# Optimization experiments

Measured on AMD Instinct MI355X. Metric: run time of the kernel, lower is better.

The kernel has to match this reference:

```python
import jax, jax.numpy as jnp
import numpy as np

OUT_CH = 300
KSIZE = 337

def setup_inputs() -> dict:
    key = jax.random.key(0)
    k1, k2, kw, kb, kf1, kb1, kf2, kb2 = jax.random.split(key, 8)
    B, W = 512, 128
    x1 = jax.random.normal(k1, (B, W, KSIZE), dtype=jnp.float32)
    x2 = jax.random.normal(k2, (B, W, KSIZE), dtype=jnp.float32)
    # Conv1d(1, 300, 337) weight [300, 1, 337] -> collapse to [300, 337]
    conv_w = jax.random.normal(kw, (OUT_CH, KSIZE), dtype=jnp.float32) * (1.0 / np.sqrt(KSIZE))
    conv_b = jax.random.normal(kb, (OUT_CH,), dtype=jnp.float32) * 0.01
    fc1_w = jax.random.normal(kf1, (300, 600), dtype=jnp.float32) * (1.0 / np.sqrt(600))
    fc1_b = jax.random.normal(kb1, (300,), dtype=jnp.float32) * 0.01
    fc2_w = jax.random.normal(kf2, (1, 300), dtype=jnp.float32) * (1.0 / np.sqrt(300))
    fc2_b = jax.random.normal(kb2, (1,), dtype=jnp.float32) * 0.01
    return {"x1": x1, "x2": x2, "conv_w": conv_w, "conv_b": conv_b,
            "fc1_w": fc1_w, "fc1_b": fc1_b, "fc2_w": fc2_w, "fc2_b": fc2_b}

def _encode(x, conv_w, conv_b):
    # per-word conv1d with full-length kernel == matmul over last dim
    # x: [B, W, 337] -> [B, W, 300] -> relu -> max over words -> [B, 300]
    h = jnp.einsum('bwd,od->bwo', x, conv_w) + conv_b
    h = jax.nn.relu(h)
    return jnp.max(h, axis=1)

def reference(x1, x2, conv_w, conv_b, fc1_w, fc1_b, fc2_w, fc2_b):
    v1 = _encode(x1, conv_w, conv_b)
    v2 = _encode(x2, conv_w, conv_b)
    feat = jnp.concatenate([v1 - v2, v1 * v2], axis=1)  # [B, 600]
    h = jnp.tanh(feat @ fc1_w.T + fc1_b)
    return h @ fc2_w.T + fc2_b  # [B, 1]
```

## Files before the change

### kernel.cpp

```cpp
#include <hip/hip_runtime.h>
#include <hip/hip_fp16.h>
#include <stdint.h>


#define OC   300
#define OCP  320
#define KD   337
#define KDP  352
#define NBAT 512
#define NWRD 128
#define NKT  11

typedef _Float16 f16x8 __attribute__((ext_vector_type(8)));
typedef float    f32x4 __attribute__((ext_vector_type(4)));

__global__ void prep_w_kernel(const float* __restrict__ cw, __half* __restrict__ W16) {
  int i = blockIdx.x * 256 + threadIdx.x;
  if (i >= OCP * KDP) return;
  int o = i / KDP, d = i - o * KDP;
  float v = (o < OC && d < KD) ? cw[o * KD + d] : 0.f;
  W16[i] = __float2half(v);
}

__global__ void prep_fc1t_kernel(const float* __restrict__ w, float* __restrict__ T) {
  int i = blockIdx.x * 256 + threadIdx.x;
  if (i >= 300 * 600) return;
  int j = i / 600, k = i - j * 600;
  T[k * 300 + j] = w[i];
}

__device__ __forceinline__ uint4 pack8h(const float* f) {
  uint4 u;
  u.x = ((uint32_t)__half_as_ushort(__float2half(f[1])) << 16) | (uint32_t)__half_as_ushort(__float2half(f[0]));
  u.y = ((uint32_t)__half_as_ushort(__float2half(f[3])) << 16) | (uint32_t)__half_as_ushort(__float2half(f[2]));
  u.z = ((uint32_t)__half_as_ushort(__float2half(f[5])) << 16) | (uint32_t)__half_as_ushort(__float2half(f[4]));
  u.w = ((uint32_t)__half_as_ushort(__float2half(f[7])) << 16) | (uint32_t)__half_as_ushort(__float2half(f[6]));
  return u;
}

__global__ __launch_bounds__(512) void encode_gemm(
    const float* __restrict__ x1, const float* __restrict__ x2,
    const __half* __restrict__ W16, const float* __restrict__ cb,
    float* __restrict__ V)
{
  __shared__ uint4 At[2][512];
  __shared__ float colmax[2][OCP];

  const int tid  = threadIdx.x;
  const int lane = tid & 63;
  const int wid  = tid >> 6;
  const int wm   = wid >> 2;
  const int wn   = wid & 3;
  const int ib   = blockIdx.x;
  const float* xb = (ib < NBAT ? x1 : x2) + (size_t)(ib & (NBAT - 1)) * (NWRD * KD);

  const int srow  = tid >> 2;
  const int sseg  = tid & 3;
  const int sslot = (srow * 4 + sseg) ^ (srow & 7);
  const float* sp = xb + srow * KD + sseg * 8;

  f32x4 acc[4][5];
  #pragma unroll
  for (int mi = 0; mi < 4; ++mi)
    #pragma unroll
    for (int ni = 0; ni < 5; ++ni)
      acc[mi][ni] = (f32x4){0.f, 0.f, 0.f, 0.f};

  {
    float f[8];
    #pragma unroll
    for (int j = 0; j < 8; ++j) f[j] = sp[j];
    At[0][sslot] = pack8h(f);
  }
  __syncthreads();

  for (int kt = 0; kt < NKT; ++kt) {
    const int cur = kt & 1;

    float f[8];
    if (kt < NKT - 1) {
      const int dbase = (kt + 1) * 32 + sseg * 8;
      const float* p  = sp + (kt + 1) * 32;
      if (dbase + 8 <= KD) {
        #pragma unroll
        for (int j = 0; j < 8; ++j) f[j] = p[j];
      } else {
        #pragma unroll
        for (int j = 0; j < 8; ++j) f[j] = (dbase + j < KD) ? p[j] : 0.f;
      }
    }

    f16x8 a[4];
    #pragma unroll
    for (int mi = 0; mi < 4; ++mi) {
      int r    = wm * 64 + mi * 16 + (lane & 15);
      int slot = (r * 4 + (lane >> 4)) ^ (r & 7);
      a[mi] = *reinterpret_cast<const f16x8*>(&At[cur][slot]);
    }
    f16x8 b[5];
    #pragma unroll
    for (int ni = 0; ni < 5; ++ni) {
      int o = wn * 80 + ni * 16 + (lane & 15);
      b[ni] = *reinterpret_cast<const f16x8*>(W16 + (size_t)o * KDP + kt * 32 + (lane >> 4) * 8);
    }

    #pragma unroll
    for (int mi = 0; mi < 4; ++mi)
      #pragma unroll
      for (int ni = 0; ni < 5; ++ni)
        acc[mi][ni] = __builtin_amdgcn_mfma_f32_16x16x32_f16(a[mi], b[ni], acc[mi][ni], 0, 0, 0);

    if (kt < NKT - 1) {
      At[cur ^ 1][sslot] = pack8h(f);
    }
    __syncthreads();
  }

  #pragma unroll
  for (int ni = 0; ni < 5; ++ni) {
    float m = acc[0][ni][0];
    #pragma unroll
    for (int mi = 0; mi < 4; ++mi)
      #pragma unroll
      for (int j = 0; j < 4; ++j)
        m = fmaxf(m, acc[mi][ni][j]);
    m = fmaxf(m, __shfl_xor(m, 16));
    m = fmaxf(m, __shfl_xor(m, 32));
    if (lane < 16) colmax[wm][wn * 80 + ni * 16 + lane] = m;
  }
  __syncthreads();
  if (tid < OCP) {
    float v = fmaxf(colmax[0][tid], colmax[1][tid]);
    if (tid < OC) V[(size_t)ib * OC + tid] = fmaxf(v + cb[tid], 0.f);
  }
}

__global__ __launch_bounds__(320) void head_kernel(
    const float* __restrict__ V, const float* __restrict__ T,
    const float* __restrict__ fc1b, const float* __restrict__ fc2w,
    const float* __restrict__ fc2b, float* __restrict__ out)
{
  __shared__ float feat[8][600];
  __shared__ float partial[8][5];
  const int tid  = threadIdx.x;
  const int lane = tid & 63;
  const int wid  = tid >> 6;
  const int b0   = blockIdx.x * 8;

  for (int idx = tid; idx < 8 * 600; idx += 320) {
    int q = idx / 600, k = idx - q * 600;
    int b = b0 + q;
    int c = (k < 300) ? k : k - 300;
    float a1 = V[(size_t)b * OC + c];
    float a2 = V[(size_t)(NBAT + b) * OC + c];
    feat[q][k] = (k < 300) ? (a1 - a2) : (a1 * a2);
  }
  __syncthreads();

  const int j = tid;
  float h[8] = {0.f, 0.f, 0.f, 0.f, 0.f, 0.f, 0.f, 0.f};
  if (j < 300) {
    for (int k4 = 0; k4 < 150; ++k4) {
      float w0 = T[(k4 * 4 + 0) * 300 + j];
      float w1 = T[(k4 * 4 + 1) * 300 + j];
      float w2 = T[(k4 * 4 + 2) * 300 + j];
      float w3 = T[(k4 * 4 + 3) * 300 + j];
      #pragma unroll
      for (int q = 0; q < 8; ++q) {
        float4 fv = *reinterpret_cast<const float4*>(&feat[q][k4 * 4]);
        h[q] = fmaf(fv.x, w0, h[q]);
        h[q] = fmaf(fv.y, w1, h[q]);
        h[q] = fmaf(fv.z, w2, h[q]);
        h[q] = fmaf(fv.w, w3, h[q]);
      }
    }
  }
  float bias = (j < 300) ? fc1b[j] : 0.f;
  float w2j  = (j < 300) ? fc2w[j] : 0.f;
  #pragma unroll
  for (int q = 0; q < 8; ++q) {
    float g = (j < 300) ? tanhf(h[q] + bias) * w2j : 0.f;
    #pragma unroll
    for (int s = 1; s < 64; s <<= 1) g += __shfl_xor(g, s);
    if (lane == 0) partial[q][wid] = g;
  }
  __syncthreads();
  if (tid < 8) {
    float s = fc2b[0];
    #pragma unroll
    for (int wv = 0; wv < 5; ++wv) s += partial[tid][wv];
    out[b0 + tid] = s;
  }
}

extern "C" void kernel_launch(void* const* d_in, const int* in_sizes, int n_in,
                              void* d_out, int out_size, void* d_ws, size_t ws_size,
                              hipStream_t stream) {
  const float* x1     = (const float*)d_in[0];
  const float* x2     = (const float*)d_in[1];
  const float* conv_w = (const float*)d_in[2];
  const float* conv_b = (const float*)d_in[3];
  const float* fc1_w  = (const float*)d_in[4];
  const float* fc1_b  = (const float*)d_in[5];
  const float* fc2_w  = (const float*)d_in[6];
  const float* fc2_b  = (const float*)d_in[7];
  float* out = (float*)d_out;

  uint8_t* ws = (uint8_t*)d_ws;
  __half* W16 = (__half*)ws;
  float*  V   = (float*)(ws + 225280);
  float*  T   = (float*)(ws + 225280 + 1228800);

  prep_w_kernel<<<(OCP * KDP + 255) / 256, 256, 0, stream>>>(conv_w, W16);
  prep_fc1t_kernel<<<(300 * 600 + 255) / 256, 256, 0, stream>>>(fc1_w, T);
  encode_gemm<<<1024, 512, 0, stream>>>(x1, x2, W16, conv_b, V);
  head_kernel<<<64, 320, 0, stream>>>(V, T, fc1_b, fc2_w, fc2_b, out);
}
```

Before: 286.7 us.

## Stage weights in LDS, persist blocks over four items, pipeline loads across items

Each block now handles four batch items in sequence, giving 256 blocks instead of 1024. The conv weights are staged into a swizzled LDS double buffer, where before they were read straight from global memory by every wave. The x loads switch to coalesced column-strided per-lane reads, and the next tile's loads, including across item boundaries, are prefetched during the MFMA of the current tile. This aims to cut redundant global weight traffic and per-block launch and prologue costs. In exchange it uses more LDS per block and launches fewer blocks, which lowers parallelism on a 256-CU device.

After: 307.9 us. +7.4%, slower.

```diff
diff --git a/kernel.cpp b/kernel.cpp
--- a/kernel.cpp
+++ b/kernel.cpp
@@ -10,6 +10,7 @@
 #define NBAT 512
 #define NWRD 128
 #define NKT  11
+#define IPB  4
 
 typedef _Float16 f16x8 __attribute__((ext_vector_type(8)));
 typedef float    f32x4 __attribute__((ext_vector_type(4)));
@@ -29,21 +30,13 @@
   T[k * 300 + j] = w[i];
 }
 
-__device__ __forceinline__ uint4 pack8h(const float* f) {
-  uint4 u;
-  u.x = ((uint32_t)__half_as_ushort(__float2half(f[1])) << 16) | (uint32_t)__half_as_ushort(__float2half(f[0]));
-  u.y = ((uint32_t)__half_as_ushort(__float2half(f[3])) << 16) | (uint32_t)__half_as_ushort(__float2half(f[2]));
-  u.z = ((uint32_t)__half_as_ushort(__float2half(f[5])) << 16) | (uint32_t)__half_as_ushort(__float2half(f[4]));
-  u.w = ((uint32_t)__half_as_ushort(__float2half(f[7])) << 16) | (uint32_t)__half_as_ushort(__float2half(f[6]));
-  return u;
-}
-
 __global__ __launch_bounds__(512) void encode_gemm(
     const float* __restrict__ x1, const float* __restrict__ x2,
     const __half* __restrict__ W16, const float* __restrict__ cb,
     float* __restrict__ V)
 {
-  __shared__ uint4 At[2][512];
+  __shared__ uint4 Bt[2][1280];
+  __shared__ uint4 Xt[2][512];
   __shared__ float colmax[2][OCP];
 
   const int tid  = threadIdx.x;
@@ -51,13 +44,41 @@
   const int wid  = tid >> 6;
   const int wm   = wid >> 2;
   const int wn   = wid & 3;
-  const int ib   = blockIdx.x;
-  const float* xb = (ib < NBAT ? x1 : x2) + (size_t)(ib & (NBAT - 1)) * (NWRD * KD);
-
-  const int srow  = tid >> 2;
-  const int sseg  = tid & 3;
-  const int sslot = (srow * 4 + sseg) ^ (srow & 7);
-  const float* sp = xb + srow * KD + sseg * 8;
+
+  const int sx   = tid & 31;
+  const int rgrp = tid >> 5;
+
+  const int ib0 = blockIdx.x * IPB;
+
+  float xf[8];
+  uint4 bf0, bf1, bf2;
+
+  auto ISSUE = [&](int item, int kt) {
+    int ib = ib0 + item;
+    const float* xb = (ib < NBAT ? x1 : x2) + (size_t)(ib & (NBAT - 1)) * (NWRD * KD);
+    const float* xp = xb + rgrp * 8 * KD + kt * 32 + sx;
+    bool ok = (kt < NKT - 1) || (sx < KD - 320);
+    #pragma unroll
+    for (int rr = 0; rr < 8; ++rr) xf[rr] = ok ? xp[rr * KD] : 0.f;
+    const __half* wp = W16 + kt * 32;
+    bf0 = *reinterpret_cast<const uint4*>(wp + (size_t)(tid >> 2) * KDP + (tid & 3) * 8);
+    { int g = tid + 512;  bf1 = *reinterpret_cast<const uint4*>(wp + (size_t)(g >> 2) * KDP + (g & 3) * 8); }
+    if (tid < 256) { int g = tid + 1024; bf2 = *reinterpret_cast<const uint4*>(wp + (size_t)(g >> 2) * KDP + (g & 3) * 8); }
+  };
+
+  auto WRITE = [&](int buf) {
+    __half* Xh = reinterpret_cast<__half*>(&Xt[buf][0]);
+    #pragma unroll
+    for (int rr = 0; rr < 8; ++rr) {
+      int r    = rgrp * 8 + rr;
+      int slot = (r * 4 + (sx >> 3)) ^ (r & 7);
+      Xh[slot * 8 + (sx & 7)] = __float2half(xf[rr]);
+    }
+    uint4* Bb = &Bt[buf][0];
+    { int g = tid;        Bb[g ^ ((g >> 2) & 7)] = bf0; }
+    { int g = tid + 512;  Bb[g ^ ((g >> 2) & 7)] = bf1; }
+    if (tid < 256) { int g = tid + 1024; Bb[g ^ ((g >> 2) & 7)] = bf2; }
+  };
 
   f32x4 acc[4][5];
   #pragma unroll
@@ -66,72 +87,66 @@
     for (int ni = 0; ni < 5; ++ni)
       acc[mi][ni] = (f32x4){0.f, 0.f, 0.f, 0.f};
 
-  {
-    float f[8];
-    #pragma unroll
-    for (int j = 0; j < 8; ++j) f[j] = sp[j];
-    At[0][sslot] = pack8h(f);
-  }
+  ISSUE(0, 0);
+  WRITE(0);
   __syncthreads();
 
-  for (int kt = 0; kt < NKT; ++kt) {
-    const int cur = kt & 1;
-
-    float f[8];
-    if (kt < NKT - 1) {
-      const int dbase = (kt + 1) * 32 + sseg * 8;
-      const float* p  = sp + (kt + 1) * 32;
-      if (dbase + 8 <= KD) {
+  int cur = 0;
+  for (int item = 0; item < IPB; ++item) {
+    for (int kt = 0; kt < NKT; ++kt) {
+      int inext = item, knext = kt + 1;
+      if (knext == NKT) { knext = 0; inext = (item + 1 < IPB) ? item + 1 : item; }
+      ISSUE(inext, knext);
+
+      f16x8 a[4], b[5];
+      #pragma unroll
+      for (int mi = 0; mi < 4; ++mi) {
+        int r    = wm * 64 + mi * 16 + (lane & 15);
+        int slot = (r * 4 + (lane >> 4)) ^ (r & 7);
+        a[mi] = *reinterpret_cast<const f16x8*>(&Xt[cur][slot]);
+      }
+      #pragma unroll
+      for (int ni = 0; ni < 5; ++ni) {
+        int o    = wn * 80 + ni * 16 + (lane & 15);
+        int slot = (o * 4 + (lane >> 4)) ^ (o & 7);
+        b[ni] = *reinterpret_cast<const f16x8*>(&Bt[cur][slot]);
+      }
+
+      #pragma unroll
+      for (int mi = 0; mi < 4; ++mi)
         #pragma unroll
-        for (int j = 0; j < 8; ++j) f[j] = p[j];
-      } else {
+        for (int ni = 0; ni < 5; ++ni)
+          acc[mi][ni] = __builtin_amdgcn_mfma_f32_16x16x32_f16(a[mi], b[ni], acc[mi][ni], 0, 0, 0);
+
+      WRITE(cur ^ 1);
+
+      if (kt == NKT - 1) {
         #pragma unroll
-        for (int j = 0; j < 8; ++j) f[j] = (dbase + j < KD) ? p[j] : 0.f;
-      }
+        for (int ni = 0; ni < 5; ++ni) {
+          float m = acc[0][ni][0];
+          #pragma unroll
+          for (int mi = 0; mi < 4; ++mi)
+            #pragma unroll
+            for (int j = 0; j < 4; ++j)
+              m = fmaxf(m, acc[mi][ni][j]);
+          m = fmaxf(m, __shfl_xor(m, 16));
+          m = fmaxf(m, __shfl_xor(m, 32));
+          if (lane < 16) colmax[wm][wn * 80 + ni * 16 + lane] = m;
+        }
+        __syncthreads();
+        if (tid < OCP) {
+          float v = fmaxf(colmax[0][tid], colmax[1][tid]);
+          if (tid < OC) V[(size_t)(ib0 + item) * OC + tid] = fmaxf(v + cb[tid], 0.f);
+        }
+        #pragma unroll
+        for (int mi = 0; mi < 4; ++mi)
+          #pragma unroll
+          for (int ni = 0; ni < 5; ++ni)
+            acc[mi][ni] = (f32x4){0.f, 0.f, 0.f, 0.f};
+      }
+      __syncthreads();
+      cur ^= 1;
     }
-
-    f16x8 a[4];
-    #pragma unroll
-    for (int mi = 0; mi < 4; ++mi) {
-      int r    = wm * 64 + mi * 16 + (lane & 15);
-      int slot = (r * 4 + (lane >> 4)) ^ (r & 7);
-      a[mi] = *reinterpret_cast<const f16x8*>(&At[cur][slot]);
-    }
-    f16x8 b[5];
-    #pragma unroll
-    for (int ni = 0; ni < 5; ++ni) {
-      int o = wn * 80 + ni * 16 + (lane & 15);
-      b[ni] = *reinterpret_cast<const f16x8*>(W16 + (size_t)o * KDP + kt * 32 + (lane >> 4) * 8);
-    }
-
-    #pragma unroll
-    for (int mi = 0; mi < 4; ++mi)
-      #pragma unroll
-      for (int ni = 0; ni < 5; ++ni)
-        acc[mi][ni] = __builtin_amdgcn_mfma_f32_16x16x32_f16(a[mi], b[ni], acc[mi][ni], 0, 0, 0);
-
-    if (kt < NKT - 1) {
-      At[cur ^ 1][sslot] = pack8h(f);
-    }
-    __syncthreads();
-  }
-
-  #pragma unroll
-  for (int ni = 0; ni < 5; ++ni) {
-    float m = acc[0][ni][0];
-    #pragma unroll
-    for (int mi = 0; mi < 4; ++mi)
-      #pragma unroll
-      for (int j = 0; j < 4; ++j)
-        m = fmaxf(m, acc[mi][ni][j]);
-    m = fmaxf(m, __shfl_xor(m, 16));
-    m = fmaxf(m, __shfl_xor(m, 32));
-    if (lane < 16) colmax[wm][wn * 80 + ni * 16 + lane] = m;
-  }
-  __syncthreads();
-  if (tid < OCP) {
-    float v = fmaxf(colmax[0][tid], colmax[1][tid]);
-    if (tid < OC) V[(size_t)ib * OC + tid] = fmaxf(v + cb[tid], 0.f);
   }
 }
 
@@ -213,6 +228,6 @@
 
   prep_w_kernel<<<(OCP * KDP + 255) / 256, 256, 0, stream>>>(conv_w, W16);
   prep_fc1t_kernel<<<(300 * 600 + 255) / 256, 256, 0, stream>>>(fc1_w, T);
-  encode_gemm<<<1024, 512, 0, stream>>>(x1, x2, W16, conv_b, V);
+  encode_gemm<<<256, 512, 0, stream>>>(x1, x2, W16, conv_b, V);
   head_kernel<<<64, 320, 0, stream>>>(V, T, fc1_b, fc2_w, fc2_b, out);
 }
```

## Stream X and weight tiles into LDS via async global_load_lds double buffering

Applied to the files above, without the earlier changes.

Replaces the register-staged fp32 loads, fp16 packing and LDS stores of the activation tile with direct global-to-LDS async loads of raw fp32 (4-byte per element, padded stride 36). The fp32-to-fp16 conversion moves to the LDS read side. Conv weights are pre-tiled and swizzled per k-tile so they are also copied into LDS asynchronously instead of being read from global memory per wave. The goal is to overlap the next tile's loads with MFMA work and cut register and VALU traffic, at the cost of more LDS (about 77KB) and many small 4-byte load instructions.

Measured after the change: 333.3 us. 16.3% more time.

```diff
diff --git a/kernel.cpp b/kernel.cpp
--- a/kernel.cpp
+++ b/kernel.cpp
@@ -6,20 +6,36 @@
 #define OC   300
 #define OCP  320
 #define KD   337
-#define KDP  352
 #define NBAT 512
 #define NWRD 128
 #define NKT  11
+#define XSTR 36
+#define XDW  (NWRD * XSTR)
+#define BGR  1280
 
 typedef _Float16 f16x8 __attribute__((ext_vector_type(8)));
 typedef float    f32x4 __attribute__((ext_vector_type(4)));
 
-__global__ void prep_w_kernel(const float* __restrict__ cw, __half* __restrict__ W16) {
+#define GL_LDS(gp, lp, SZ)                                                        \
+  __builtin_amdgcn_global_load_lds(                                               \
+      (const __attribute__((address_space(1))) uint32_t*)(gp),                    \
+      (__attribute__((address_space(3))) uint32_t*)(lp), SZ, 0, 0)
+
+__global__ void prep_w_kernel(const float* __restrict__ cw, __half* __restrict__ Wp) {
   int i = blockIdx.x * 256 + threadIdx.x;
-  if (i >= OCP * KDP) return;
-  int o = i / KDP, d = i - o * KDP;
-  float v = (o < OC && d < KD) ? cw[o * KD + d] : 0.f;
-  W16[i] = __float2half(v);
+  if (i >= NKT * BGR) return;
+  int kt = i / BGR, lin = i - kt * BGR;
+  int o = lin >> 2, g = lin & 3;
+  int slot = lin ^ (o & 7);
+  __half h[8];
+  #pragma unroll
+  for (int e = 0; e < 8; ++e) {
+    int k = kt * 32 + g * 8 + e;
+    float v = (o < OC && k < KD) ? cw[o * KD + k] : 0.f;
+    h[e] = __float2half(v);
+  }
+  *reinterpret_cast<uint4*>(Wp + (size_t)(kt * BGR + slot) * 8) =
+      *reinterpret_cast<const uint4*>(h);
 }
 
 __global__ void prep_fc1t_kernel(const float* __restrict__ w, float* __restrict__ T) {
@@ -29,21 +45,13 @@
   T[k * 300 + j] = w[i];
 }
 
-__device__ __forceinline__ uint4 pack8h(const float* f) {
-  uint4 u;
-  u.x = ((uint32_t)__half_as_ushort(__float2half(f[1])) << 16) | (uint32_t)__half_as_ushort(__float2half(f[0]));
-  u.y = ((uint32_t)__half_as_ushort(__float2half(f[3])) << 16) | (uint32_t)__half_as_ushort(__float2half(f[2]));
-  u.z = ((uint32_t)__half_as_ushort(__float2half(f[5])) << 16) | (uint32_t)__half_as_ushort(__float2half(f[4]));
-  u.w = ((uint32_t)__half_as_ushort(__float2half(f[7])) << 16) | (uint32_t)__half_as_ushort(__float2half(f[6]));
-  return u;
-}
-
-__global__ __launch_bounds__(512) void encode_gemm(
+__global__ __launch_bounds__(512, 4) void encode_gemm(
     const float* __restrict__ x1, const float* __restrict__ x2,
-    const __half* __restrict__ W16, const float* __restrict__ cb,
+    const __half* __restrict__ Wp, const float* __restrict__ cb,
     float* __restrict__ V)
 {
-  __shared__ uint4 At[2][512];
+  __shared__ float Xt[2][XDW];
+  __shared__ uint4 Bt[2][BGR];
   __shared__ float colmax[2][OCP];
 
   const int tid  = threadIdx.x;
@@ -54,10 +62,29 @@
   const int ib   = blockIdx.x;
   const float* xb = (ib < NBAT ? x1 : x2) + (size_t)(ib & (NBAT - 1)) * (NWRD * KD);
 
-  const int srow  = tid >> 2;
-  const int sseg  = tid & 3;
-  const int sslot = (srow * 4 + sseg) ^ (srow & 7);
-  const float* sp = xb + srow * KD + sseg * 8;
+  int rk[9];
+  #pragma unroll
+  for (int j = 0; j < 9; ++j) {
+    int s = j * 512 + tid;
+    int r = s / XSTR, k = s - r * XSTR;
+    rk[j] = (r << 8) | ((k < 32) ? k : 31);
+  }
+
+  #define ISSUE(KT, BUF) do {                                                        \
+    const int kt_ = (KT);                                                            \
+    const int ko_ = kt_ * 32;                                                        \
+    _Pragma("unroll")                                                                \
+    for (int j = 0; j < 9; ++j) {                                                    \
+      int r_ = rk[j] >> 8, kc_ = rk[j] & 255;                                        \
+      int gk_ = ko_ + kc_; gk_ = (gk_ > KD - 1) ? (KD - 1) : gk_;    \
+      GL_LDS(xb + (size_t)r_ * KD + gk_, &Xt[BUF][j * 512 + tid], 4);                \
+    }                                                                                \
+    const __half* wsrc_ = Wp + (size_t)kt_ * BGR * 8;                                \
+    GL_LDS(wsrc_ + (size_t)tid * 8,          &Bt[BUF][tid],        16);              \
+    GL_LDS(wsrc_ + (size_t)(tid + 512) * 8,  &Bt[BUF][tid + 512],  16);              \
+    if (tid < 256)                                                                   \
+      GL_LDS(wsrc_ + (size_t)(tid + 1024) * 8, &Bt[BUF][tid + 1024], 16);            \
+  } while (0)
 
   f32x4 acc[4][5];
   #pragma unroll
@@ -66,53 +93,40 @@
     for (int ni = 0; ni < 5; ++ni)
       acc[mi][ni] = (f32x4){0.f, 0.f, 0.f, 0.f};
 
-  {
-    float f[8];
-    #pragma unroll
-    for (int j = 0; j < 8; ++j) f[j] = sp[j];
-    At[0][sslot] = pack8h(f);
-  }
-  __syncthreads();
-
+  ISSUE(0, 0);
+  asm volatile("s_waitcnt vmcnt(0)" ::: "memory");
+  __syncthreads();
+
+  const int k0 = (lane >> 4) * 8;
   for (int kt = 0; kt < NKT; ++kt) {
     const int cur = kt & 1;
-
-    float f[8];
-    if (kt < NKT - 1) {
-      const int dbase = (kt + 1) * 32 + sseg * 8;
-      const float* p  = sp + (kt + 1) * 32;
-      if (dbase + 8 <= KD) {
-        #pragma unroll
-        for (int j = 0; j < 8; ++j) f[j] = p[j];
-      } else {
-        #pragma unroll
-        for (int j = 0; j < 8; ++j) f[j] = (dbase + j < KD) ? p[j] : 0.f;
-      }
+    if (kt + 1 < NKT) ISSUE(kt + 1, cur ^ 1);
+
+    f16x8 a[4];
+    #pragma unroll
+    for (int mi = 0; mi < 4; ++mi) {
+      int r = wm * 64 + mi * 16 + (lane & 15);
+      const float* xp = &Xt[cur][r * XSTR + k0];
+      f32x4 lo = *reinterpret_cast<const f32x4*>(xp);
+      f32x4 hi = *reinterpret_cast<const f32x4*>(xp + 4);
+      f16x8 v;
+      v[0] = (_Float16)lo[0]; v[1] = (_Float16)lo[1];
+      v[2] = (_Float16)lo[2]; v[3] = (_Float16)lo[3];
+      v[4] = (_Float16)hi[0]; v[5] = (_Float16)hi[1];
+      v[6] = (_Float16)hi[2]; v[7] = (_Float16)hi[3];
+      a[mi] = v;
     }
-
-    f16x8 a[4];
-    #pragma unroll
-    for (int mi = 0; mi < 4; ++mi) {
-      int r    = wm * 64 + mi * 16 + (lane & 15);
-      int slot = (r * 4 + (lane >> 4)) ^ (r & 7);
-      a[mi] = *reinterpret_cast<const f16x8*>(&At[cur][slot]);
+    #pragma unroll
+    for (int ni = 0; ni < 5; ++ni) {
+      int o    = wn * 80 + ni * 16 + (lane & 15);
+      int slot = (o * 4 + (lane >> 4)) ^ (o & 7);
+      f16x8 b = *reinterpret_cast<const f16x8*>(&Bt[cur][slot]);
+      #pragma unroll
+      for (int mi = 0; mi < 4; ++mi)
+        acc[mi][ni] = __builtin_amdgcn_mfma_f32_16x16x32_f16(a[mi], b, acc[mi][ni], 0, 0, 0);
     }
-    f16x8 b[5];
-    #pragma unroll
-    for (int ni = 0; ni < 5; ++ni) {
-      int o = wn * 80 + ni * 16 + (lane & 15);
-      b[ni] = *reinterpret_cast<const f16x8*>(W16 + (size_t)o * KDP + kt * 32 + (lane >> 4) * 8);
-    }
-
-    #pragma unroll
-    for (int mi = 0; mi < 4; ++mi)
-      #pragma unroll
-      for (int ni = 0; ni < 5; ++ni)
-        acc[mi][ni] = __builtin_amdgcn_mfma_f32_16x16x32_f16(a[mi], b[ni], acc[mi][ni], 0, 0, 0);
-
-    if (kt < NKT - 1) {
-      At[cur ^ 1][sslot] = pack8h(f);
-    }
+
+    asm volatile("s_waitcnt vmcnt(0)" ::: "memory");
     __syncthreads();
   }
 
@@ -207,12 +221,12 @@
   float* out = (float*)d_out;
 
   uint8_t* ws = (uint8_t*)d_ws;
-  __half* W16 = (__half*)ws;
-  float*  V   = (float*)(ws + 225280);
-  float*  T   = (float*)(ws + 225280 + 1228800);
-
-  prep_w_kernel<<<(OCP * KDP + 255) / 256, 256, 0, stream>>>(conv_w, W16);
+  __half* Wp = (__half*)ws;
+  float*  V  = (float*)(ws + 225280);
+  float*  T  = (float*)(ws + 225280 + 1228800);
+
+  prep_w_kernel<<<(NKT * BGR + 255) / 256, 256, 0, stream>>>(conv_w, Wp);
   prep_fc1t_kernel<<<(300 * 600 + 255) / 256, 256, 0, stream>>>(fc1_w, T);
-  encode_gemm<<<1024, 512, 0, stream>>>(x1, x2, W16, conv_b, V);
+  encode_gemm<<<1024, 512, 0, stream>>>(x1, x2, Wp, conv_b, V);
   head_kernel<<<64, 320, 0, stream>>>(V, T, fc1_b, fc2_w, fc2_b, out);
 }
```
